# Performance work log

Hardware: AMD Instinct MI355X
Metric: run time of the kernel (lower is better)

The kernel has to match this reference:

```python
import jax, jax.numpy as jnp
import numpy as np

EPS = 1e-12  # torch F.normalize eps


def setup_inputs() -> dict:
    key = jax.random.key(0)
    k1, k2, k3 = jax.random.split(key, 3)
    N, C, H, W = 64, 512, 30, 30
    K = 64
    x = jax.random.normal(k1, (N, C, H, W), dtype=jnp.float32)
    # 1x1 conv weight [K, C] (kernel spatial dims squeezed out)
    conv_w = jax.random.normal(k2, (K, C), dtype=jnp.float32) * 0.04
    centroids = jax.random.uniform(k3, (K, C), dtype=jnp.float32)
    return {"x": x, "conv_w": conv_w, "centroids": centroids}


def reference(x, conv_w, centroids):
    N, C, H, W = x.shape
    K = conv_w.shape[0]
    # descriptor-wise L2 normalize over channel dim (normalize_input=True)
    nrm = jnp.sqrt(jnp.sum(x * x, axis=1, keepdims=True))
    x = x / jnp.maximum(nrm, EPS)
    xf = x.reshape(N, C, H * W)                       # [N, C, P]
    # 1x1 conv == per-pixel matmul: [N, K, P]
    logits = jnp.einsum("kc,ncp->nkp", conv_w, xf)
    a = jax.nn.softmax(logits, axis=1)                # softmax over clusters
    # vlad[n,k,c] = sum_p a[n,k,p] * (xf[n,c,p] - centroids[k,c])
    #            = (a @ xf^T) - sum_p(a) * centroids   (GEMM decomposition)
    agg = jnp.einsum("nkp,ncp->nkc", a, xf)           # [N, K, C]
    vlad = agg - a.sum(axis=-1)[:, :, None] * centroids[None]
    return vlad
```

## Files before the change

### kernel.cpp

```cpp
#include <hip/hip_runtime.h>
#include <math.h>

#define N_DIM 64
#define C_DIM 512
#define K_DIM 64
#define P_DIM 900
#define P_PAD 928
#define PTILES 15
#define CTILES 8

typedef __attribute__((ext_vector_type(8))) short short8;
typedef __attribute__((ext_vector_type(4))) float f32x4;
typedef __attribute__((ext_vector_type(4))) uint  u32x4;

#define A2_ELEMS   ((size_t)N_DIM * K_DIM * P_PAD)
#define ASUM_ELEMS ((size_t)N_DIM * K_DIM * PTILES)
#define SSQ_ELEMS  ((size_t)CTILES * N_DIM * P_DIM)
#define XTF_ELEMS  ((size_t)N_DIM * PTILES * 16 * 4 * 64 * 8)

__device__ inline ushort f2bf(float f) {
  uint u = __builtin_bit_cast(uint, f);
  u += 0x7FFFu + ((u >> 16) & 1u);
  return (ushort)(u >> 16);
}
__device__ inline uint pk2(float a, float b) {
  return (uint)f2bf(a) | ((uint)f2bf(b) << 16);
}

__global__ __launch_bounds__(256) void transpose_x(
    const float* __restrict__ x, ushort* __restrict__ xtf,
    float* __restrict__ ssq_part)
{
  const int ct = blockIdx.x, pt = blockIdx.y, n = blockIdx.z;
  const int p0 = pt * 64, c0 = ct * 64, tid = threadIdx.x;
  __shared__ float lds[64][68];
  __shared__ float red[4][64];

  const float* xb = x + ((size_t)n * C_DIM + c0) * P_DIM;
  const int cl = tid >> 4;
  const int p4 = (tid & 15) * 4;
#pragma unroll
  for (int pass = 0; pass < 4; ++pass) {
    const int c = cl + pass * 16;
    const int gp = p0 + p4;
    float4 v;
    if (gp + 4 <= P_DIM) {
      v = *(const float4*)(xb + (size_t)c * P_DIM + gp);
    } else {
      v.x = (gp + 0 < P_DIM) ? xb[(size_t)c * P_DIM + gp + 0] : 0.f;
      v.y = (gp + 1 < P_DIM) ? xb[(size_t)c * P_DIM + gp + 1] : 0.f;
      v.z = (gp + 2 < P_DIM) ? xb[(size_t)c * P_DIM + gp + 2] : 0.f;
      v.w = (gp + 3 < P_DIM) ? xb[(size_t)c * P_DIM + gp + 3] : 0.f;
    }
    *(float4*)&lds[c][p4] = v;
  }
  __syncthreads();

  const int pl = tid & 63, co = tid >> 6;
  float ssq = 0.f;
  uint pk[8];
#pragma unroll
  for (int q = 0; q < 8; ++q) {
    float a = lds[co * 16 + q * 2 + 0][pl];
    float b = lds[co * 16 + q * 2 + 1][pl];
    ssq += a * a + b * b;
    pk[q] = pk2(a, b);
  }
  red[co][pl] = ssq;

  const size_t fbase = ((size_t)n * PTILES + pt) * 16;
#pragma unroll
  for (int o = 0; o < 2; ++o) {
    const int cg = c0 + co * 16 + o * 8;
    const int ks  = cg >> 5;
    const int lhi = (cg >> 3) & 3;
    u32x4 wv;
    wv[0] = pk[o * 4 + 0]; wv[1] = pk[o * 4 + 1];
    wv[2] = pk[o * 4 + 2]; wv[3] = pk[o * 4 + 3];
    *(u32x4*)(xtf + (((fbase + ks) * 4 + lhi) * 64 + pl) * 8) = wv;
  }
  __syncthreads();
  if (tid < 64) {
    int p = p0 + tid;
    if (p < P_DIM)
      ssq_part[((size_t)ct * N_DIM + n) * P_DIM + p] =
          red[0][tid] + red[1][tid] + red[2][tid] + red[3][tid];
  }
}

__global__ __launch_bounds__(256, 2) void netvlad_assign(
    const float* __restrict__ w, const ushort* __restrict__ xtf,
    const float* __restrict__ ssq_part,
    ushort* __restrict__ a2, float* __restrict__ asum_part)
{
  const int n = blockIdx.y, bpt = blockIdx.x, p0 = bpt * 64;
  const int tid = threadIdx.x, wave = tid >> 6, lane = tid & 63;
  const int l15 = lane & 15, lhi = lane >> 4;

  __shared__ float invn_s[64];
  __shared__ float wredm[4][4][16];
  __shared__ float wreds[4][4][16];

  short8 wfrag[16];
  const float* wrow = w + (size_t)(wave * 16 + l15) * C_DIM + lhi * 8;
#pragma unroll
  for (int ks = 0; ks < 16; ++ks) {
    f32x4 f0 = *(const f32x4*)(wrow + ks * 32);
    f32x4 f1 = *(const f32x4*)(wrow + ks * 32 + 4);
    u32x4 up;
    up[0] = pk2(f0[0], f0[1]); up[1] = pk2(f0[2], f0[3]);
    up[2] = pk2(f1[0], f1[1]); up[3] = pk2(f1[2], f1[3]);
    wfrag[ks] = __builtin_bit_cast(short8, up);
  }

  if (tid < 64) {
    int p = p0 + tid;
    float s = 0.f;
    if (p < P_DIM) {
#pragma unroll
      for (int ct = 0; ct < CTILES; ++ct)
        s += ssq_part[((size_t)ct * N_DIM + n) * P_DIM + p];
    }
    invn_s[tid] = 1.0f / fmaxf(sqrtf(s), 1e-12f);
  }

  const ushort* xf_base = xtf + ((size_t)n * PTILES + bpt) * 16 * 4 * 64 * 8;
  f32x4 acc[4];
#pragma unroll
  for (int pt = 0; pt < 4; ++pt) acc[pt] = (f32x4){0.f, 0.f, 0.f, 0.f};

#pragma unroll
  for (int ks = 0; ks < 16; ++ks) {
#pragma unroll
    for (int pt = 0; pt < 4; ++pt) {
      short8 xf = *(const short8*)(xf_base
                    + (((size_t)ks * 4 + lhi) * 64 + pt * 16 + l15) * 8);
      acc[pt] = __builtin_amdgcn_mfma_f32_16x16x32_bf16(wfrag[ks], xf, acc[pt], 0, 0, 0);
    }
  }
  __syncthreads();

  float linv[4], lg[4][4];
#pragma unroll
  for (int pt = 0; pt < 4; ++pt) {
    linv[pt] = invn_s[pt * 16 + l15];
    float m = -1e30f;
#pragma unroll
    for (int r = 0; r < 4; ++r) { lg[pt][r] = acc[pt][r] * linv[pt]; m = fmaxf(m, lg[pt][r]); }
    m = fmaxf(m, __shfl_xor(m, 16));
    m = fmaxf(m, __shfl_xor(m, 32));
    if (lhi == 0) wredm[wave][pt][l15] = m;
  }
  __syncthreads();
#pragma unroll
  for (int pt = 0; pt < 4; ++pt) {
    float m = fmaxf(fmaxf(wredm[0][pt][l15], wredm[1][pt][l15]),
                    fmaxf(wredm[2][pt][l15], wredm[3][pt][l15]));
    float s = 0.f;
#pragma unroll
    for (int r = 0; r < 4; ++r) { lg[pt][r] = __expf(lg[pt][r] - m); s += lg[pt][r]; }
    s += __shfl_xor(s, 16);
    s += __shfl_xor(s, 32);
    if (lhi == 0) wreds[wave][pt][l15] = s;
  }
  __syncthreads();

  ushort* a2b = a2 + (size_t)n * K_DIM * P_PAD;
  float asr[4] = {0.f, 0.f, 0.f, 0.f};
#pragma unroll
  for (int pt = 0; pt < 4; ++pt) {
    float stot = wreds[0][pt][l15] + wreds[1][pt][l15] +
                 wreds[2][pt][l15] + wreds[3][pt][l15];
    float rs = 1.0f / stot;
    int p = p0 + pt * 16 + l15;
    bool vv = p < P_DIM;
#pragma unroll
    for (int r = 0; r < 4; ++r) {
      float a = lg[pt][r] * rs;
      if (vv) asr[r] += a;
      if (p < P_PAD) {
        int k = wave * 16 + lhi * 4 + r;
        a2b[(size_t)k * P_PAD + p] = vv ? f2bf(a * linv[pt]) : (ushort)0;
      }
    }
  }
#pragma unroll
  for (int r = 0; r < 4; ++r) {
    float v = asr[r];
    v += __shfl_xor(v, 1); v += __shfl_xor(v, 2);
    v += __shfl_xor(v, 4); v += __shfl_xor(v, 8);
    if (l15 == 0) {
      int k = wave * 16 + lhi * 4 + r;
      asum_part[((size_t)n * K_DIM + k) * PTILES + bpt] = v;
    }
  }
}

__global__ __launch_bounds__(256, 4) void netvlad_agg(
    const float* __restrict__ x, const ushort* __restrict__ a2,
    const float* __restrict__ asum_part, const float* __restrict__ cent,
    float* __restrict__ out)
{
  const int n = blockIdx.y, ct = blockIdx.x, c0 = ct * 64;
  const int tid = threadIdx.x, wave = tid >> 6, lane = tid & 63;
  const int l15 = lane & 15, lhi = lane >> 4;

  __shared__ float asum_s[64];
  if (tid < 64) {
    const float* ap = asum_part + ((size_t)n * K_DIM + tid) * PTILES;
    float s = 0.f;
#pragma unroll
    for (int j = 0; j < PTILES; ++j) s += ap[j];
    asum_s[tid] = s;
  }
  __syncthreads();

  f32x4 acc[4];
#pragma unroll
  for (int mt = 0; mt < 4; ++mt) acc[mt] = (f32x4){0.f, 0.f, 0.f, 0.f};

  const float*  xrow = x + (size_t)n * C_DIM * P_DIM
                         + (size_t)(c0 + wave * 16 + l15) * P_DIM;
  const ushort* ab   = a2 + (size_t)n * K_DIM * P_PAD;

  for (int ks = 0; ks < 29; ++ks) {
    int pb = ks * 32 + lhi * 8;
    short8 bfrag;
    if (pb + 8 <= P_DIM) {
      f32x4 f0 = *(const f32x4*)(xrow + pb);
      f32x4 f1 = *(const f32x4*)(xrow + pb + 4);
      u32x4 up;
      up[0] = pk2(f0[0], f0[1]); up[1] = pk2(f0[2], f0[3]);
      up[2] = pk2(f1[0], f1[1]); up[3] = pk2(f1[2], f1[3]);
      bfrag = __builtin_bit_cast(short8, up);
    } else {
#pragma unroll
      for (int j = 0; j < 8; ++j)
        bfrag[j] = (pb + j < P_DIM) ? (short)f2bf(xrow[pb + j]) : (short)0;
    }
#pragma unroll
    for (int mt = 0; mt < 4; ++mt) {
      short8 afrag = *(const short8*)(ab + (size_t)(mt * 16 + l15) * P_PAD
                                         + ks * 32 + lhi * 8);
      acc[mt] = __builtin_amdgcn_mfma_f32_16x16x32_bf16(afrag, bfrag, acc[mt], 0, 0, 0);
    }
  }

  const int c = c0 + wave * 16 + l15;
#pragma unroll
  for (int mt = 0; mt < 4; ++mt) {
#pragma unroll
    for (int r = 0; r < 4; ++r) {
      int k = mt * 16 + lhi * 4 + r;
      out[((size_t)n * K_DIM + k) * C_DIM + c] =
          acc[mt][r] - asum_s[k] * cent[(size_t)k * C_DIM + c];
    }
  }
}

extern "C" void kernel_launch(void* const* d_in, const int* in_sizes, int n_in,
                              void* d_out, int out_size, void* d_ws, size_t ws_size,
                              hipStream_t stream) {
  const float* x    = (const float*)d_in[0];
  const float* w    = (const float*)d_in[1];
  const float* cent = (const float*)d_in[2];
  float* out = (float*)d_out;

  char* wsb = (char*)d_ws;
  ushort* a2        = (ushort*)wsb;
  float*  asum_part = (float*)(wsb + A2_ELEMS * sizeof(ushort));
  float*  ssq_part  = asum_part + ASUM_ELEMS;
  ushort* xtf       = (ushort*)((char*)(ssq_part + SSQ_ELEMS));

  transpose_x   <<<dim3(CTILES, PTILES, N_DIM), 256, 0, stream>>>(x, xtf, ssq_part);
  netvlad_assign<<<dim3(PTILES, N_DIM),         256, 0, stream>>>(w, xtf, ssq_part, a2, asum_part);
  netvlad_agg   <<<dim3(CTILES, N_DIM),         256, 0, stream>>>(x, a2, asum_part, cent, out);
}
```

Baseline: 91.35 us.

## Restructure transpose kernel into double-buffered global-to-LDS pipeline over channel slabs

The transpose/ssq kernel now runs one block per (channel tile, image) covering all 900 pixels, instead of one block per 64x64 tile. It streams 8-channel slabs into a double-buffered LDS array using direct global_load_lds and explicit waitcnt and barriers, so loads overlap with bf16 packing. Each thread keeps its sum-of-squares partials in registers across slabs rather than doing a block reduction per tile. This cuts the block count sharply, which lowers launch and per-tile overhead, but leaves far fewer waves in flight per CU to hide memory latency. The xtf layout is unchanged and only the index expressions in the consumer are rewritten.

```diff
diff --git a/kernel.cpp b/kernel.cpp
--- a/kernel.cpp
+++ b/kernel.cpp
@@ -7,7 +7,6 @@
 #define P_DIM 900
 #define P_PAD 928
 #define PTILES 15
-#define CTILES 8
 
 typedef __attribute__((ext_vector_type(8))) short short8;
 typedef __attribute__((ext_vector_type(4))) float f32x4;
@@ -15,8 +14,8 @@
 
 #define A2_ELEMS   ((size_t)N_DIM * K_DIM * P_PAD)
 #define ASUM_ELEMS ((size_t)N_DIM * K_DIM * PTILES)
-#define SSQ_ELEMS  ((size_t)CTILES * N_DIM * P_DIM)
-#define XTF_ELEMS  ((size_t)N_DIM * PTILES * 16 * 4 * 64 * 8)
+#define SSQ_ELEMS  ((size_t)8 * N_DIM * P_DIM)
+#define XTF_ELEMS  ((size_t)N_DIM * PTILES * 16 * 4 * 512)
 
 __device__ inline ushort f2bf(float f) {
   uint u = __builtin_bit_cast(uint, f);
@@ -26,65 +25,81 @@
 __device__ inline uint pk2(float a, float b) {
   return (uint)f2bf(a) | ((uint)f2bf(b) << 16);
 }
-
-__global__ __launch_bounds__(256) void transpose_x(
+__device__ __forceinline__ void gload16(const float* g, float* lds_base) {
+  __builtin_amdgcn_global_load_lds(
+      (const __attribute__((address_space(1))) void*)g,
+      (__attribute__((address_space(3))) void*)lds_base, 16, 0, 0);
+}
+
+__global__ __launch_bounds__(256, 2) void transpose_x(
     const float* __restrict__ x, ushort* __restrict__ xtf,
     float* __restrict__ ssq_part)
 {
-  const int ct = blockIdx.x, pt = blockIdx.y, n = blockIdx.z;
-  const int p0 = pt * 64, c0 = ct * 64, tid = threadIdx.x;
-  __shared__ float lds[64][68];
-  __shared__ float red[4][64];
-
-  const float* xb = x + ((size_t)n * C_DIM + c0) * P_DIM;
-  const int cl = tid >> 4;
-  const int p4 = (tid & 15) * 4;
+  const int ct = blockIdx.x, n = blockIdx.y, c0 = ct * 64;
+  const int tid = threadIdx.x, wv = tid >> 6, lane = tid & 63;
+
+  __shared__ float xs[2][8192];
+
+  const float* xb = x + (size_t)n * C_DIM * P_DIM;
+#define STAGE(b, it)                                                           \
+  {                                                                            \
+    _Pragma("unroll")                                                          \
+    for (int i = 0; i < 8; ++i) {                                              \
+      int j = wv * 8 + i;                                                      \
+      int r = j >> 2, q = j & 3;                                               \
+      int px = q * 256 + lane * 4;                                             \
+      if (px > 896) px = 896;                                                  \
+      gload16(xb + (size_t)(c0 + (it) * 8 + r) * P_DIM + px,                   \
+              &xs[b][r * 1024 + q * 256]);                                     \
+    }                                                                          \
+  }
+
+  float ssq_acc[4] = {0.f, 0.f, 0.f, 0.f};
+
+  STAGE(0, 0);
+#pragma unroll
+  for (int it = 0; it < 8; ++it) {
+    if (it + 1 < 8) STAGE((it + 1) & 1, it + 1);
+    if (it + 1 < 8) asm volatile("s_waitcnt vmcnt(8)" ::: "memory");
+    else            asm volatile("s_waitcnt vmcnt(0)" ::: "memory");
+    __builtin_amdgcn_sched_barrier(0);
+    __builtin_amdgcn_s_barrier();
+
+    const float* buf = xs[it & 1];
+    const int cg = c0 + it * 8;
+    const int ks = cg >> 5, lhi = (cg >> 3) & 3;
+    ushort* dst_base = xtf + (((size_t)(n * PTILES) * 16 + ks) * 4 + lhi) * 512;
+#pragma unroll
+    for (int pass = 0; pass < 4; ++pass) {
+      int px = pass * 256 + tid;
+      float v[8];
+#pragma unroll
+      for (int c = 0; c < 8; ++c) v[c] = buf[c * 1024 + px];
+      if (px >= P_DIM) {
+#pragma unroll
+        for (int c = 0; c < 8; ++c) v[c] = 0.f;
+      }
+      float s = 0.f;
+#pragma unroll
+      for (int c = 0; c < 8; ++c) s += v[c] * v[c];
+      ssq_acc[pass] += s;
+      if (px < PTILES * 64) {
+        int pt = px >> 6, pxl = px & 63;
+        u32x4 wvr;
+        wvr[0] = pk2(v[0], v[1]); wvr[1] = pk2(v[2], v[3]);
+        wvr[2] = pk2(v[4], v[5]); wvr[3] = pk2(v[6], v[7]);
+        *(u32x4*)(dst_base + (size_t)pt * 16 * 4 * 512 + pxl * 8) = wvr;
+      }
+    }
+    __builtin_amdgcn_s_barrier();
+  }
+#undef STAGE
+
 #pragma unroll
   for (int pass = 0; pass < 4; ++pass) {
-    const int c = cl + pass * 16;
-    const int gp = p0 + p4;
-    float4 v;
-    if (gp + 4 <= P_DIM) {
-      v = *(const float4*)(xb + (size_t)c * P_DIM + gp);
-    } else {
-      v.x = (gp + 0 < P_DIM) ? xb[(size_t)c * P_DIM + gp + 0] : 0.f;
-      v.y = (gp + 1 < P_DIM) ? xb[(size_t)c * P_DIM + gp + 1] : 0.f;
-      v.z = (gp + 2 < P_DIM) ? xb[(size_t)c * P_DIM + gp + 2] : 0.f;
-      v.w = (gp + 3 < P_DIM) ? xb[(size_t)c * P_DIM + gp + 3] : 0.f;
-    }
-    *(float4*)&lds[c][p4] = v;
-  }
-  __syncthreads();
-
-  const int pl = tid & 63, co = tid >> 6;
-  float ssq = 0.f;
-  uint pk[8];
-#pragma unroll
-  for (int q = 0; q < 8; ++q) {
-    float a = lds[co * 16 + q * 2 + 0][pl];
-    float b = lds[co * 16 + q * 2 + 1][pl];
-    ssq += a * a + b * b;
-    pk[q] = pk2(a, b);
-  }
-  red[co][pl] = ssq;
-
-  const size_t fbase = ((size_t)n * PTILES + pt) * 16;
-#pragma unroll
-  for (int o = 0; o < 2; ++o) {
-    const int cg = c0 + co * 16 + o * 8;
-    const int ks  = cg >> 5;
-    const int lhi = (cg >> 3) & 3;
-    u32x4 wv;
-    wv[0] = pk[o * 4 + 0]; wv[1] = pk[o * 4 + 1];
-    wv[2] = pk[o * 4 + 2]; wv[3] = pk[o * 4 + 3];
-    *(u32x4*)(xtf + (((fbase + ks) * 4 + lhi) * 64 + pl) * 8) = wv;
-  }
-  __syncthreads();
-  if (tid < 64) {
-    int p = p0 + tid;
-    if (p < P_DIM)
-      ssq_part[((size_t)ct * N_DIM + n) * P_DIM + p] =
-          red[0][tid] + red[1][tid] + red[2][tid] + red[3][tid];
+    int px = pass * 256 + tid;
+    if (px < P_DIM)
+      ssq_part[((size_t)ct * N_DIM + n) * P_DIM + px] = ssq_acc[pass];
   }
 }
 
@@ -118,13 +133,13 @@
     float s = 0.f;
     if (p < P_DIM) {
 #pragma unroll
-      for (int ct = 0; ct < CTILES; ++ct)
+      for (int ct = 0; ct < 8; ++ct)
         s += ssq_part[((size_t)ct * N_DIM + n) * P_DIM + p];
     }
     invn_s[tid] = 1.0f / fmaxf(sqrtf(s), 1e-12f);
   }
 
-  const ushort* xf_base = xtf + ((size_t)n * PTILES + bpt) * 16 * 4 * 64 * 8;
+  const ushort* xf_base = xtf + ((size_t)(n * PTILES + bpt) * 16) * 4 * 512;
   f32x4 acc[4];
 #pragma unroll
   for (int pt = 0; pt < 4; ++pt) acc[pt] = (f32x4){0.f, 0.f, 0.f, 0.f};
@@ -133,8 +148,8 @@
   for (int ks = 0; ks < 16; ++ks) {
 #pragma unroll
     for (int pt = 0; pt < 4; ++pt) {
-      short8 xf = *(const short8*)(xf_base
-                    + (((size_t)ks * 4 + lhi) * 64 + pt * 16 + l15) * 8);
+      short8 xf = *(const short8*)(xf_base + ((size_t)ks * 4 + lhi) * 512
+                                          + (pt * 16 + l15) * 8);
       acc[pt] = __builtin_amdgcn_mfma_f32_16x16x32_bf16(wfrag[ks], xf, acc[pt], 0, 0, 0);
     }
   }
@@ -272,7 +287,7 @@
   float*  ssq_part  = asum_part + ASUM_ELEMS;
   ushort* xtf       = (ushort*)((char*)(ssq_part + SSQ_ELEMS));
 
-  transpose_x   <<<dim3(CTILES, PTILES, N_DIM), 256, 0, stream>>>(x, xtf, ssq_part);
-  netvlad_assign<<<dim3(PTILES, N_DIM),         256, 0, stream>>>(w, xtf, ssq_part, a2, asum_part);
-  netvlad_agg   <<<dim3(CTILES, N_DIM),         256, 0, stream>>>(x, a2, asum_part, cent, out);
-}
+  transpose_x   <<<dim3(8, N_DIM),      256, 0, stream>>>(x, xtf, ssq_part);
+  netvlad_assign<<<dim3(PTILES, N_DIM), 256, 0, stream>>>(w, xtf, ssq_part, a2, asum_part);
+  netvlad_agg   <<<dim3(8, N_DIM),      256, 0, stream>>>(x, a2, asum_part, cent, out);
+}
```

Measured after the change: 97.39 us. 6.6% more time.
